# Performance work log

Measured on AMD Instinct MI355X. Metric: run time of the kernel, lower is better.

## Reference

```python
import jax, jax.numpy as jnp
import numpy as np

N_NODES = 100000
N_EDGES = 2000000
F_IN = 32
HID = 32
N_CLASS = 40


def _gru_cell(m, h, wih, whh, bih, bhh):
    # torch.nn.GRUCell math; wih/whh: [3H, H_in], gates ordered r, z, n
    gi = m @ wih.T + bih
    gh = h @ whh.T + bhh
    i_r, i_z, i_n = jnp.split(gi, 3, axis=-1)
    h_r, h_z, h_n = jnp.split(gh, 3, axis=-1)
    r = jax.nn.sigmoid(i_r + h_r)
    z = jax.nn.sigmoid(i_z + h_z)
    n = jnp.tanh(i_n + r * h_n)
    return (1.0 - z) * n + z * h


def _gated_conv(x, edge_index, edge_weight, w_proj, w_msg, wih, whh, bih, bhh):
    h = x @ w_proj                                   # [N, out]
    msg = (h @ w_msg)[edge_index[0]] * edge_weight[:, None]  # gather src -> [E, out]
    agg = jax.ops.segment_sum(msg, edge_index[1], num_segments=N_NODES)  # scatter-add to dst
    return _gru_cell(agg, h, wih, whh, bih, bhh)


def setup_inputs() -> dict:
    key = jax.random.key(0)
    ks = jax.random.split(key, 16)
    s = 0.1
    return {
        "x": jax.random.normal(ks[0], (N_NODES, F_IN), jnp.float32),
        "edge_index": jax.random.randint(ks[1], (2, N_EDGES), 0, N_NODES, jnp.int64),
        "edge_weight": jax.random.uniform(ks[2], (N_EDGES,), jnp.float32),
        "W1_proj": jax.random.normal(ks[3], (F_IN, HID), jnp.float32) * s,
        "W1_msg": jax.random.normal(ks[4], (HID, HID), jnp.float32) * s,
        "gru1_wih": jax.random.normal(ks[5], (3 * HID, HID), jnp.float32) * s,
        "gru1_whh": jax.random.normal(ks[6], (3 * HID, HID), jnp.float32) * s,
        "gru1_bih": jax.random.normal(ks[7], (3 * HID,), jnp.float32) * s,
        "gru1_bhh": jax.random.normal(ks[8], (3 * HID,), jnp.float32) * s,
        "W2_proj": jax.random.normal(ks[9], (HID, N_CLASS), jnp.float32) * s,
        "W2_msg": jax.random.normal(ks[10], (N_CLASS, N_CLASS), jnp.float32) * s,
        "gru2_wih": jax.random.normal(ks[11], (3 * N_CLASS, N_CLASS), jnp.float32) * s,
        "gru2_whh": jax.random.normal(ks[12], (3 * N_CLASS, N_CLASS), jnp.float32) * s,
        "gru2_bih": jax.random.normal(ks[13], (3 * N_CLASS,), jnp.float32) * s,
        "gru2_bhh": jax.random.normal(ks[14], (3 * N_CLASS,), jnp.float32) * s,
    }


def reference(x, edge_index, edge_weight, W1_proj, W1_msg, gru1_wih, gru1_whh,
              gru1_bih, gru1_bhh, W2_proj, W2_msg, gru2_wih, gru2_whh,
              gru2_bih, gru2_bhh):
    # eval mode: dropout is identity
    h = _gated_conv(x, edge_index, edge_weight, W1_proj, W1_msg,
                    gru1_wih, gru1_whh, gru1_bih, gru1_bhh)
    h = jax.nn.relu(h)
    h = _gated_conv(h, edge_index, edge_weight, W2_proj, W2_msg,
                    gru2_wih, gru2_whh, gru2_bih, gru2_bhh)
    return jax.nn.log_softmax(h, axis=-1)
```

## Files before the change

kernel.cpp:

```cpp
#include <hip/hip_runtime.h>
#include <math.h>

#define NN 100000
#define NE 2000000
#define FIN 32
#define H 32
#define NC 40

#define NBK 196
#define BSH 9
#define CAP 10880
#define EPT 16
#define EPB (256 * EPT)

#define NPROJ 12500
#define NCT1 10
#define NCT2 12
#define NWB 118

typedef _Float16 half_t;
typedef __attribute__((ext_vector_type(8))) _Float16 half8;
typedef __attribute__((ext_vector_type(4))) float f32x4;
typedef long long ll2 __attribute__((ext_vector_type(2)));

__device__ __forceinline__ float sigm_(float x) {
    return 1.0f / (1.0f + __expf(-x));
}
__device__ __forceinline__ float tanh_(float x) {
    x = fminf(fmaxf(x, -20.0f), 20.0f);
    float e = __expf(2.0f * x);
    return (e - 1.0f) / (e + 1.0f);
}

__device__ __forceinline__ void agg_run(int e, int e1, int q,
                                        const int2* __restrict__ evs,
                                        const half_t* __restrict__ src,
                                        float* acc) {
    const half8* s8 = (const half8*)src + q;
    const long long* ev8 = (const long long*)evs;
    if ((e & 1) && e < e1) {
        long long r = __builtin_nontemporal_load(ev8 + e);
        float w = __int_as_float((int)(r >> 32));
        half8 hv = s8[(size_t)(r & 0x1FFFF) * 4];
#pragma unroll
        for (int t = 0; t < 8; ++t) acc[t] += w * (float)hv[t];
        ++e;
    }
    int nfull = (e1 - e) >> 3;
    if (nfull > 0) {
        ll2 p0 = __builtin_nontemporal_load((const ll2*)(ev8 + e));
        ll2 p1 = __builtin_nontemporal_load((const ll2*)(ev8 + e + 2));
        ll2 p2 = __builtin_nontemporal_load((const ll2*)(ev8 + e + 4));
        ll2 p3 = __builtin_nontemporal_load((const ll2*)(ev8 + e + 6));
        for (int it = 1; it < nfull; ++it) {
            int en = e + it * 8;
            ll2 q0 = __builtin_nontemporal_load((const ll2*)(ev8 + en));
            ll2 q1 = __builtin_nontemporal_load((const ll2*)(ev8 + en + 2));
            ll2 q2 = __builtin_nontemporal_load((const ll2*)(ev8 + en + 4));
            ll2 q3 = __builtin_nontemporal_load((const ll2*)(ev8 + en + 6));
            half8 h0 = s8[(size_t)(p0[0] & 0x1FFFF) * 4];
            half8 h1 = s8[(size_t)(p0[1] & 0x1FFFF) * 4];
            half8 h2 = s8[(size_t)(p1[0] & 0x1FFFF) * 4];
            half8 h3 = s8[(size_t)(p1[1] & 0x1FFFF) * 4];
            half8 h4 = s8[(size_t)(p2[0] & 0x1FFFF) * 4];
            half8 h5 = s8[(size_t)(p2[1] & 0x1FFFF) * 4];
            half8 h6 = s8[(size_t)(p3[0] & 0x1FFFF) * 4];
            half8 h7 = s8[(size_t)(p3[1] & 0x1FFFF) * 4];
            float w0 = __int_as_float((int)(p0[0] >> 32));
            float w1 = __int_as_float((int)(p0[1] >> 32));
            float w2 = __int_as_float((int)(p1[0] >> 32));
            float w3 = __int_as_float((int)(p1[1] >> 32));
            float w4 = __int_as_float((int)(p2[0] >> 32));
            float w5 = __int_as_float((int)(p2[1] >> 32));
            float w6 = __int_as_float((int)(p3[0] >> 32));
            float w7 = __int_as_float((int)(p3[1] >> 32));
#pragma unroll
            for (int t = 0; t < 8; ++t) {
                acc[t] += w0 * (float)h0[t];
                acc[t] += w1 * (float)h1[t];
                acc[t] += w2 * (float)h2[t];
                acc[t] += w3 * (float)h3[t];
                acc[t] += w4 * (float)h4[t];
                acc[t] += w5 * (float)h5[t];
                acc[t] += w6 * (float)h6[t];
                acc[t] += w7 * (float)h7[t];
            }
            p0 = q0;
            p1 = q1;
            p2 = q2;
            p3 = q3;
        }
        {
            half8 h0 = s8[(size_t)(p0[0] & 0x1FFFF) * 4];
            half8 h1 = s8[(size_t)(p0[1] & 0x1FFFF) * 4];
            half8 h2 = s8[(size_t)(p1[0] & 0x1FFFF) * 4];
            half8 h3 = s8[(size_t)(p1[1] & 0x1FFFF) * 4];
            half8 h4 = s8[(size_t)(p2[0] & 0x1FFFF) * 4];
            half8 h5 = s8[(size_t)(p2[1] & 0x1FFFF) * 4];
            half8 h6 = s8[(size_t)(p3[0] & 0x1FFFF) * 4];
            half8 h7 = s8[(size_t)(p3[1] & 0x1FFFF) * 4];
            float w0 = __int_as_float((int)(p0[0] >> 32));
            float w1 = __int_as_float((int)(p0[1] >> 32));
            float w2 = __int_as_float((int)(p1[0] >> 32));
            float w3 = __int_as_float((int)(p1[1] >> 32));
            float w4 = __int_as_float((int)(p2[0] >> 32));
            float w5 = __int_as_float((int)(p2[1] >> 32));
            float w6 = __int_as_float((int)(p3[0] >> 32));
            float w7 = __int_as_float((int)(p3[1] >> 32));
#pragma unroll
            for (int t = 0; t < 8; ++t) {
                acc[t] += w0 * (float)h0[t];
                acc[t] += w1 * (float)h1[t];
                acc[t] += w2 * (float)h2[t];
                acc[t] += w3 * (float)h3[t];
                acc[t] += w4 * (float)h4[t];
                acc[t] += w5 * (float)h5[t];
                acc[t] += w6 * (float)h6[t];
                acc[t] += w7 * (float)h7[t];
            }
        }
        e += nfull * 8;
    }
    if (e + 4 <= e1) {
        ll2 p0 = __builtin_nontemporal_load((const ll2*)(ev8 + e));
        ll2 p1 = __builtin_nontemporal_load((const ll2*)(ev8 + e + 2));
        half8 h0 = s8[(size_t)(p0[0] & 0x1FFFF) * 4];
        half8 h1 = s8[(size_t)(p0[1] & 0x1FFFF) * 4];
        half8 h2 = s8[(size_t)(p1[0] & 0x1FFFF) * 4];
        half8 h3 = s8[(size_t)(p1[1] & 0x1FFFF) * 4];
        float w0 = __int_as_float((int)(p0[0] >> 32));
        float w1 = __int_as_float((int)(p0[1] >> 32));
        float w2 = __int_as_float((int)(p1[0] >> 32));
        float w3 = __int_as_float((int)(p1[1] >> 32));
#pragma unroll
        for (int t = 0; t < 8; ++t) {
            acc[t] += w0 * (float)h0[t];
            acc[t] += w1 * (float)h1[t];
            acc[t] += w2 * (float)h2[t];
            acc[t] += w3 * (float)h3[t];
        }
        e += 4;
    }
    if (e + 2 <= e1) {
        ll2 p0 = __builtin_nontemporal_load((const ll2*)(ev8 + e));
        half8 h0 = s8[(size_t)(p0[0] & 0x1FFFF) * 4];
        half8 h1 = s8[(size_t)(p0[1] & 0x1FFFF) * 4];
        float w0 = __int_as_float((int)(p0[0] >> 32));
        float w1 = __int_as_float((int)(p0[1] >> 32));
#pragma unroll
        for (int t = 0; t < 8; ++t) {
            acc[t] += w0 * (float)h0[t];
            acc[t] += w1 * (float)h1[t];
        }
        e += 2;
    }
    if (e < e1) {
        long long r = __builtin_nontemporal_load(ev8 + e);
        float w = __int_as_float((int)(r >> 32));
        half8 hv = s8[(size_t)(r & 0x1FFFF) * 4];
#pragma unroll
        for (int t = 0; t < 8; ++t) acc[t] += w * (float)hv[t];
    }
}

__global__ __launch_bounds__(256) void kA_bucket(const int* __restrict__ ei,
                                                 const float* __restrict__ ew,
                                                 int* __restrict__ gcur,
                                                 long long* __restrict__ rec) {
    __shared__ long long recs[EPB];
    __shared__ int gdst[EPB];
    __shared__ int cnt[NBK], base[NBK], sofs[NBK];
    __shared__ int ssc[256];
    int tid = threadIdx.x;
    for (int i = tid; i < NBK; i += 256) cnt[i] = 0;
    __syncthreads();
    int e0 = blockIdx.x * EPB;
    int dcache[EPT];
#pragma unroll
    for (int i = 0; i < EPT; ++i) {
        int e = e0 + i * 256 + tid;
        dcache[i] = (e < NE) ? ei[NE + e] : -1;
        if (e < NE) atomicAdd(&cnt[dcache[i] >> BSH], 1);
    }
    __syncthreads();
    int cv = (tid < NBK) ? cnt[tid] : 0;
    ssc[tid] = cv;
    __syncthreads();
    for (int off = 1; off < 256; off <<= 1) {
        int v = (tid >= off) ? ssc[tid - off] : 0;
        __syncthreads();
        ssc[tid] += v;
        __syncthreads();
    }
    if (tid < NBK) {
        sofs[tid] = ssc[tid] - cv;
        base[tid] = atomicAdd(&gcur[tid], cv);
        cnt[tid] = 0;
    }
    __syncthreads();
#pragma unroll
    for (int i = 0; i < EPT; ++i) {
        int e = e0 + i * 256 + tid;
        if (e < NE) {
            int d = dcache[i], s = ei[e];
            int b = d >> BSH;
            int r = atomicAdd(&cnt[b], 1);
            int slot = sofs[b] + r;
            int pos = base[b] + r;
            int lo = s | ((d & 511) << 17);
            recs[slot] = (long long)(unsigned)lo |
                         ((long long)__float_as_int(ew[e]) << 32);
            gdst[slot] = (pos < CAP) ? (b * CAP + pos) : -1;
        }
    }
    __syncthreads();
    int nrec = min(EPB, NE - e0);
    for (int i = tid; i < nrec; i += 256) {
        int gd = gdst[i];
        if (gd >= 0) rec[gd] = recs[i];
    }
}

__global__ __launch_bounds__(256) void kB_sort(const int* __restrict__ gcur,
                                               const int2* __restrict__ rec,
                                               int2* __restrict__ evs,
                                               int* __restrict__ ofs,
                                               int* __restrict__ ocn) {
    __shared__ int hist[2048], lofs[2048], ssc[256];
    int tid = threadIdx.x, b = blockIdx.x;
    int nb0 = b << BSH;
    int nnodes = min(512, NN - nb0);
    int cntb = min(gcur[b], CAP);
    for (int i = tid; i < 2048; i += 256) hist[i] = 0;
    __syncthreads();
    const int2* rb = rec + (size_t)b * CAP;
    for (int i = tid; i < cntb; i += 256) {
        int rx = rb[i].x;
        int bin = (((rx >> 17) & 511) << 2) | ((rx & 0x1FFFF) >> 15);
        atomicAdd(&hist[bin], 1);
    }
    __syncthreads();
    int base = tid * 8, ls = 0, lh[8];
#pragma unroll
    for (int j = 0; j < 8; ++j) {
        lh[j] = hist[base + j];
        ls += lh[j];
    }
    ssc[tid] = ls;
    __syncthreads();
    for (int off = 1; off < 256; off <<= 1) {
        int v = (tid >= off) ? ssc[tid - off] : 0;
        __syncthreads();
        ssc[tid] += v;
        __syncthreads();
    }
    int ex = ssc[tid] - ls;
#pragma unroll
    for (int j = 0; j < 8; ++j) {
        lofs[base + j] = ex;
        ex += lh[j];
    }
    __syncthreads();
    for (int l = tid; l < nnodes; l += 256) {
        int c = hist[4 * l] + hist[4 * l + 1] + hist[4 * l + 2] + hist[4 * l + 3];
        ofs[nb0 + l] = b * CAP + lofs[4 * l];
        ocn[nb0 + l] = c;
    }
    __syncthreads();
    for (int i = tid; i < 2048; i += 256) hist[i] = 0;
    __syncthreads();
    int2* eb = evs + (size_t)b * CAP;
    for (int i = tid; i < cntb; i += 256) {
        int2 r = rb[i];
        int bin = (((r.x >> 17) & 511) << 2) | ((r.x & 0x1FFFF) >> 15);
        int rk = atomicAdd(&hist[bin], 1);
        eb[lofs[bin] + rk] = make_int2(r.x & 0x1FFFF, r.y);
    }
}

__global__ __launch_bounds__(256) void k_prep(const float* __restrict__ x,
                                              const float* __restrict__ W1p,
                                              const float* __restrict__ W1m,
                                              const float* __restrict__ wih1,
                                              const float* __restrict__ whh1,
                                              const float* __restrict__ W2p,
                                              const float* __restrict__ W2m,
                                              const float* __restrict__ wih2,
                                              const float* __restrict__ whh2,
                                              half_t* __restrict__ Hd,
                                              half_t* __restrict__ W1sw,
                                              half_t* __restrict__ W2sw,
                                              half_t* __restrict__ W2pf,
                                              int* __restrict__ gcur) {
    __shared__ float sWp[FIN * H];
    __shared__ float sx[8][FIN];
    __shared__ float P2l[32 * NC];
    int b = blockIdx.x, tid = threadIdx.x;
    if (b < NPROJ) {
        for (int i = tid; i < FIN * H; i += 256) sWp[i] = W1p[i];
        int nb = b * 8;
        int nl = tid >> 5, j = tid & 31;
        int n = nb + nl;
        if (n < NN) sx[nl][j] = x[(size_t)n * FIN + j];
        __syncthreads();
        float acc = 0.f;
#pragma unroll
        for (int k = 0; k < FIN; ++k) acc += sx[nl][k] * sWp[k * H + j];
        if (n < NN) Hd[(size_t)n * 32 + j] = (half_t)acc;
        return;
    }
    int wb = b - NPROJ;
    if (wb == 0 && tid < NBK) gcur[tid] = 0;
    if (wb < 40) {
        int i = wb * 256 + tid;
        int j = i & 7, lane = (i >> 3) & 63;
        int rest = i >> 9;
        int ct = rest % NCT1, s = rest / NCT1;
        int k = s * 32 + (lane >> 4) * 8 + j;
        int col = ct * 16 + (lane & 15);
        int g = col >> 5, jj = col & 31;
        float v = 0.f;
        if (g <= 2) {
            if (k < 32) {
                float acc = 0.f;
#pragma unroll
                for (int t = 0; t < H; ++t) acc += W1m[k * H + t] * wih1[(g * H + jj) * H + t];
                v = acc;
            } else if (g < 2) {
                v = whh1[(g * H + jj) * H + (k - 32)];
            }
        } else if (g == 3) {
            if (k >= 32) v = whh1[(2 * H + jj) * H + (k - 32)];
        } else {
            if (k >= 32 && (k - 32) == jj) v = 1.f;
        }
        W1sw[i] = (half_t)v;
    } else if (wb < 112) {
        for (int e = tid; e < 32 * NC; e += 256) {
            int k = e / NC, t = e % NC;
            float a = 0.f;
#pragma unroll
            for (int u = 0; u < NC; ++u) a += W2p[k * NC + u] * W2m[u * NC + t];
            P2l[e] = a;
        }
        __syncthreads();
        int i2 = (wb - 40) * 256 + tid;
        int j = i2 & 7, lane = (i2 >> 3) & 63;
        int rest = i2 >> 9;
        int ct = rest % NCT2, s = rest / NCT2;
        int k = s * 32 + (lane >> 4) * 8 + j;
        int col = ct * 16 + (lane & 15);
        int g = col / 48, jj = col % 48;
        float v = 0.f;
        if (jj < NC) {
            if (g <= 2) {
                if (k < 32) {
                    float acc = 0.f;
#pragma unroll
                    for (int t = 0; t < NC; ++t)
                        acc += P2l[k * NC + t] * wih2[(g * NC + jj) * NC + t];
                    v = acc;
                } else if (k < 72 && g < 2) {
                    v = whh2[(g * NC + jj) * NC + (k - 32)];
                }
            } else {
                if (k >= 32 && k < 72) v = whh2[(2 * NC + jj) * NC + (k - 32)];
            }
        }
        W2sw[i2] = (half_t)v;
    } else {
        int i3 = (wb - 112) * 256 + tid;
        int j = i3 & 7, lane = (i3 >> 3) & 63, ct = i3 >> 9;
        int k = (lane >> 4) * 8 + j;
        int col = ct * 16 + (lane & 15);
        W2pf[i3] = (half_t)((col < NC) ? W2p[k * NC + col] : 0.f);
    }
}

__global__ __launch_bounds__(128, 4) void k_l1(const int* __restrict__ ofs,
                                               const int* __restrict__ ocn,
                                               const int2* __restrict__ evs,
                                               const half_t* __restrict__ Hd,
                                               const half8* __restrict__ W1sw,
                                               const float* __restrict__ bih,
                                               const float* __restrict__ bhh,
                                               half_t* __restrict__ Hh) {
    __shared__ half8 aggT[16][9];
    int tid = threadIdx.x;
    int n0 = blockIdx.x * 16;
    half8 a1;
    if (tid < 64) a1 = ((const half8*)Hd)[(size_t)(n0 + (tid & 15)) * 4 + (tid >> 4)];
    {
        int nl = tid >> 3, s = tid & 7, g = s >> 2, q = s & 3;
        int n = n0 + nl;
        int s0 = ofs[n], c = ocn[n];
        int c0 = (c + 1) >> 1;
        int eb = g ? (s0 + c0) : s0;
        int ee = g ? (s0 + c) : (s0 + c0);
        float acc[8] = {0.f, 0.f, 0.f, 0.f, 0.f, 0.f, 0.f, 0.f};
        agg_run(eb, ee, q, evs, Hd, acc);
        half8 o;
#pragma unroll
        for (int t = 0; t < 8; ++t) o[t] = (half_t)acc[t];
        aggT[nl][s] = o;
    }
    __syncthreads();
    if (tid >= 64) return;
    int lane = tid, m16 = lane & 15, qq = lane >> 4;
    half8 pa = aggT[m16][qq], pb = aggT[m16][4 + qq];
    half8 a0;
#pragma unroll
    for (int t = 0; t < 8; ++t) a0[t] = (half_t)((float)pa[t] + (float)pb[t]);
    f32x4 macc[NCT1];
#pragma unroll
    for (int ct = 0; ct < NCT1; ++ct) macc[ct] = (f32x4){0.f, 0.f, 0.f, 0.f};
#pragma unroll
    for (int ct = 0; ct < NCT1; ++ct) {
        macc[ct] = __builtin_amdgcn_mfma_f32_16x16x32_f16(a0, W1sw[ct * 64 + lane], macc[ct], 0, 0, 0);
        macc[ct] = __builtin_amdgcn_mfma_f32_16x16x32_f16(a1, W1sw[(NCT1 + ct) * 64 + lane], macc[ct], 0, 0, 0);
    }
#pragma unroll
    for (int ct = 0; ct < 2; ++ct) {
        int j = ct * 16 + m16;
        float br = bih[j] + bhh[j];
        float bz = bih[H + j] + bhh[H + j];
        float bi = bih[2 * H + j], bh = bhh[2 * H + j];
#pragma unroll
        for (int m = 0; m < 4; ++m) {
            int node = n0 + qq * 4 + m;
            float r = sigm_(macc[ct][m] + br);
            float z = sigm_(macc[2 + ct][m] + bz);
            float ng = tanh_(macc[4 + ct][m] + bi + r * (macc[6 + ct][m] + bh));
            float hj = macc[8 + ct][m];
            float o = fmaxf((1.f - z) * ng + z * hj, 0.f);
            Hh[(size_t)node * 32 + j] = (half_t)o;
        }
    }
}

__global__ __launch_bounds__(128, 4) void k_l2(const int* __restrict__ ofs,
                                               const int* __restrict__ ocn,
                                               const int2* __restrict__ evs,
                                               const half_t* __restrict__ Hh,
                                               const half8* __restrict__ W2sw,
                                               const half8* __restrict__ W2pf,
                                               const float* __restrict__ bih,
                                               const float* __restrict__ bhh,
                                               float* __restrict__ out) {
    __shared__ half8 aggT[16][9];
    __shared__ half_t h2c[16][72];
    int tid = threadIdx.x;
    int n0 = blockIdx.x * 16;
    if (tid < 64) {
        int lane = tid, m16 = lane & 15, qq = lane >> 4;
        half8 ah = ((const half8*)Hh)[(size_t)(n0 + m16) * 4 + qq];
        f32x4 hC[3];
#pragma unroll
        for (int ct = 0; ct < 3; ++ct) hC[ct] = (f32x4){0.f, 0.f, 0.f, 0.f};
#pragma unroll
        for (int ct = 0; ct < 3; ++ct)
            hC[ct] = __builtin_amdgcn_mfma_f32_16x16x32_f16(ah, W2pf[ct * 64 + lane], hC[ct], 0, 0, 0);
#pragma unroll
        for (int ct = 0; ct < 3; ++ct)
#pragma unroll
            for (int m = 0; m < 4; ++m)
                h2c[qq * 4 + m][ct * 16 + m16] = (half_t)hC[ct][m];
    } else {
        int t2 = tid - 64;
        for (int i5 = t2; i5 < 16 * 24; i5 += 64)
            h2c[i5 / 24][48 + i5 % 24] = (half_t)0.f;
    }
    {
        int nl = tid >> 3, s = tid & 7, g = s >> 2, q = s & 3;
        int n = n0 + nl;
        int s0 = ofs[n], c = ocn[n];
        int c0 = (c + 1) >> 1;
        int eb = g ? (s0 + c0) : s0;
        int ee = g ? (s0 + c) : (s0 + c0);
        float acc[8] = {0.f, 0.f, 0.f, 0.f, 0.f, 0.f, 0.f, 0.f};
        agg_run(eb, ee, q, evs, Hh, acc);
        half8 o;
#pragma unroll
        for (int t = 0; t < 8; ++t) o[t] = (half_t)acc[t];
        aggT[nl][s] = o;
    }
    __syncthreads();
    if (tid >= 64) return;
    int lane = tid, m16 = lane & 15, qq = lane >> 4;
    half8 pa = aggT[m16][qq], pb = aggT[m16][4 + qq];
    half8 a0;
#pragma unroll
    for (int t = 0; t < 8; ++t) a0[t] = (half_t)((float)pa[t] + (float)pb[t]);
    half8 a1 = *(const half8*)&h2c[m16][qq * 8];
    half8 a2 = *(const half8*)&h2c[m16][32 + qq * 8];
    f32x4 macc[NCT2];
#pragma unroll
    for (int ct = 0; ct < NCT2; ++ct) macc[ct] = (f32x4){0.f, 0.f, 0.f, 0.f};
#pragma unroll
    for (int ct = 0; ct < NCT2; ++ct) {
        macc[ct] = __builtin_amdgcn_mfma_f32_16x16x32_f16(a0, W2sw[ct * 64 + lane], macc[ct], 0, 0, 0);
        macc[ct] = __builtin_amdgcn_mfma_f32_16x16x32_f16(a1, W2sw[(NCT2 + ct) * 64 + lane], macc[ct], 0, 0, 0);
        macc[ct] = __builtin_amdgcn_mfma_f32_16x16x32_f16(a2, W2sw[(2 * NCT2 + ct) * 64 + lane], macc[ct], 0, 0, 0);
    }
    float v[3][4];
#pragma unroll
    for (int ct = 0; ct < 3; ++ct) {
        int j = ct * 16 + m16;
        int jc = (j < NC) ? j : (NC - 1);
        float br = bih[jc] + bhh[jc];
        float bz = bih[NC + jc] + bhh[NC + jc];
        float bi = bih[2 * NC + jc], bh = bhh[2 * NC + jc];
#pragma unroll
        for (int m = 0; m < 4; ++m) {
            float r = sigm_(macc[ct][m] + br);
            float z = sigm_(macc[3 + ct][m] + bz);
            float ng = tanh_(macc[6 + ct][m] + bi + r * (macc[9 + ct][m] + bh));
            float hj = (float)h2c[qq * 4 + m][jc];
            v[ct][m] = (1.f - z) * ng + z * hj;
        }
    }
    bool v2ok = (m16 < 8);
#pragma unroll
    for (int m = 0; m < 4; ++m) {
        float mx = fmaxf(v[0][m], v[1][m]);
        if (v2ok) mx = fmaxf(mx, v[2][m]);
#pragma unroll
        for (int d = 1; d < 16; d <<= 1) mx = fmaxf(mx, __shfl_xor(mx, d));
        float se = __expf(v[0][m] - mx) + __expf(v[1][m] - mx) +
                   (v2ok ? __expf(v[2][m] - mx) : 0.f);
#pragma unroll
        for (int d = 1; d < 16; d <<= 1) se += __shfl_xor(se, d);
        float ls = mx + __logf(se);
        int node = n0 + qq * 4 + m;
        out[(size_t)node * NC + m16] = v[0][m] - ls;
        out[(size_t)node * NC + 16 + m16] = v[1][m] - ls;
        if (v2ok) out[(size_t)node * NC + 32 + m16] = v[2][m] - ls;
    }
}

extern "C" void kernel_launch(void* const* d_in, const int* in_sizes, int n_in,
                              void* d_out, int out_size, void* d_ws, size_t ws_size,
                              hipStream_t stream) {
    const float* x = (const float*)d_in[0];
    const int* ei = (const int*)d_in[1];
    const float* ew = (const float*)d_in[2];
    const float* W1p = (const float*)d_in[3];
    const float* W1m = (const float*)d_in[4];
    const float* g1wih = (const float*)d_in[5];
    const float* g1whh = (const float*)d_in[6];
    const float* g1bih = (const float*)d_in[7];
    const float* g1bhh = (const float*)d_in[8];
    const float* W2p = (const float*)d_in[9];
    const float* W2m = (const float*)d_in[10];
    const float* g2wih = (const float*)d_in[11];
    const float* g2whh = (const float*)d_in[12];
    const float* g2bih = (const float*)d_in[13];
    const float* g2bhh = (const float*)d_in[14];
    float* ws = (float*)d_ws;

    long long* rec = (long long*)ws;
    int2* evs = (int2*)(ws + 4264960);
    half_t* Hd = (half_t*)(ws + 8529920);
    half_t* Hh = (half_t*)(ws + 10130176);
    int* ofs = (int*)(ws + 11730432);
    int* ocn = (int*)(ws + 11830432);
    int* gcur = (int*)(ws + 11930432);
    half_t* W1sw = (half_t*)(ws + 11930688);
    half_t* W2sw = W1sw + 10240;
    half_t* W2pf = W2sw + 18432;
    float* out = (float*)d_out;

    k_prep<<<NPROJ + NWB, 256, 0, stream>>>(x, W1p, W1m, g1wih, g1whh,
                                            W2p, W2m, g2wih, g2whh,
                                            Hd, W1sw, W2sw, W2pf, gcur);
    kA_bucket<<<(NE + EPB - 1) / EPB, 256, 0, stream>>>(ei, ew, gcur, rec);
    kB_sort<<<NBK, 256, 0, stream>>>(gcur, (const int2*)rec, evs, ofs, ocn);
    k_l1<<<NN / 16, 128, 0, stream>>>(ofs, ocn, evs, Hd, (const half8*)W1sw,
                                      g1bih, g1bhh, Hh);
    k_l2<<<NN / 16, 128, 0, stream>>>(ofs, ocn, evs, Hh, (const half8*)W2sw,
                                      (const half8*)W2pf, g2bih, g2bhh, out);
}
```

Before: 258.3 us.

## Sort nodes by in-degree within buckets to balance aggregation blocks

kB_sort now builds a per-bucket counting sort of nodes by in-degree (capped at 63) and writes a node permutation. k_l1 and k_l2 process nodes in that permuted order, so each 16-node block handles nodes of similar degree and threads waiting on long edge lists are reduced. The cost is an extra permutation array, indirect loads for node ids, and scattered output writes that lose contiguity.

After: 286.4 us. +10.9%, slower.

```diff
diff --git a/kernel.cpp b/kernel.cpp
--- a/kernel.cpp
+++ b/kernel.cpp
@@ -225,13 +225,19 @@
                                                const int2* __restrict__ rec,
                                                int2* __restrict__ evs,
                                                int* __restrict__ ofs,
-                                               int* __restrict__ ocn) {
+                                               int* __restrict__ ocn,
+                                               int* __restrict__ perm) {
     __shared__ int hist[2048], lofs[2048], ssc[256];
+    __shared__ int dh[64], dcur[64];
     int tid = threadIdx.x, b = blockIdx.x;
     int nb0 = b << BSH;
     int nnodes = min(512, NN - nb0);
     int cntb = min(gcur[b], CAP);
     for (int i = tid; i < 2048; i += 256) hist[i] = 0;
+    if (tid < 64) {
+        dh[tid] = 0;
+        dcur[tid] = 0;
+    }
     __syncthreads();
     const int2* rb = rec + (size_t)b * CAP;
     for (int i = tid; i < cntb; i += 256) {
@@ -265,6 +271,24 @@
         int c = hist[4 * l] + hist[4 * l + 1] + hist[4 * l + 2] + hist[4 * l + 3];
         ofs[nb0 + l] = b * CAP + lofs[4 * l];
         ocn[nb0 + l] = c;
+        atomicAdd(&dh[min(c, 63)], 1);
+    }
+    __syncthreads();
+    if (tid == 0) {
+        int run = 0;
+#pragma unroll
+        for (int d = 0; d < 64; ++d) {
+            int v = dh[d];
+            dh[d] = run;
+            run += v;
+        }
+    }
+    __syncthreads();
+    for (int l = tid; l < nnodes; l += 256) {
+        int c = hist[4 * l] + hist[4 * l + 1] + hist[4 * l + 2] + hist[4 * l + 3];
+        int d = min(c, 63);
+        int r = atomicAdd(&dcur[d], 1);
+        perm[nb0 + dh[d] + r] = nb0 + l;
     }
     __syncthreads();
     for (int i = tid; i < 2048; i += 256) hist[i] = 0;
@@ -380,19 +404,22 @@
 __global__ __launch_bounds__(128, 4) void k_l1(const int* __restrict__ ofs,
                                                const int* __restrict__ ocn,
                                                const int2* __restrict__ evs,
+                                               const int* __restrict__ perm,
                                                const half_t* __restrict__ Hd,
                                                const half8* __restrict__ W1sw,
                                                const float* __restrict__ bih,
                                                const float* __restrict__ bhh,
                                                half_t* __restrict__ Hh) {
     __shared__ half8 aggT[16][9];
+    __shared__ int sperm[16];
     int tid = threadIdx.x;
     int n0 = blockIdx.x * 16;
+    if (tid < 16) sperm[tid] = perm[n0 + tid];
     half8 a1;
-    if (tid < 64) a1 = ((const half8*)Hd)[(size_t)(n0 + (tid & 15)) * 4 + (tid >> 4)];
+    if (tid < 64) a1 = ((const half8*)Hd)[(size_t)perm[n0 + (tid & 15)] * 4 + (tid >> 4)];
     {
         int nl = tid >> 3, s = tid & 7, g = s >> 2, q = s & 3;
-        int n = n0 + nl;
+        int n = perm[n0 + nl];
         int s0 = ofs[n], c = ocn[n];
         int c0 = (c + 1) >> 1;
         int eb = g ? (s0 + c0) : s0;
@@ -427,7 +454,7 @@
         float bi = bih[2 * H + j], bh = bhh[2 * H + j];
 #pragma unroll
         for (int m = 0; m < 4; ++m) {
-            int node = n0 + qq * 4 + m;
+            int node = sperm[qq * 4 + m];
             float r = sigm_(macc[ct][m] + br);
             float z = sigm_(macc[2 + ct][m] + bz);
             float ng = tanh_(macc[4 + ct][m] + bi + r * (macc[6 + ct][m] + bh));
@@ -441,6 +468,7 @@
 __global__ __launch_bounds__(128, 4) void k_l2(const int* __restrict__ ofs,
                                                const int* __restrict__ ocn,
                                                const int2* __restrict__ evs,
+                                               const int* __restrict__ perm,
                                                const half_t* __restrict__ Hh,
                                                const half8* __restrict__ W2sw,
                                                const half8* __restrict__ W2pf,
@@ -449,11 +477,13 @@
                                                float* __restrict__ out) {
     __shared__ half8 aggT[16][9];
     __shared__ half_t h2c[16][72];
+    __shared__ int sperm[16];
     int tid = threadIdx.x;
     int n0 = blockIdx.x * 16;
+    if (tid < 16) sperm[tid] = perm[n0 + tid];
     if (tid < 64) {
         int lane = tid, m16 = lane & 15, qq = lane >> 4;
-        half8 ah = ((const half8*)Hh)[(size_t)(n0 + m16) * 4 + qq];
+        half8 ah = ((const half8*)Hh)[(size_t)perm[n0 + m16] * 4 + qq];
         f32x4 hC[3];
 #pragma unroll
         for (int ct = 0; ct < 3; ++ct) hC[ct] = (f32x4){0.f, 0.f, 0.f, 0.f};
@@ -472,7 +502,7 @@
     }
     {
         int nl = tid >> 3, s = tid & 7, g = s >> 2, q = s & 3;
-        int n = n0 + nl;
+        int n = perm[n0 + nl];
         int s0 = ofs[n], c = ocn[n];
         int c0 = (c + 1) >> 1;
         int eb = g ? (s0 + c0) : s0;
@@ -531,7 +561,7 @@
 #pragma unroll
         for (int d = 1; d < 16; d <<= 1) se += __shfl_xor(se, d);
         float ls = mx + __logf(se);
-        int node = n0 + qq * 4 + m;
+        int node = sperm[qq * 4 + m];
         out[(size_t)node * NC + m16] = v[0][m] - ls;
         out[(size_t)node * NC + 16 + m16] = v[1][m] - ls;
         if (v2ok) out[(size_t)node * NC + 32 + m16] = v[2][m] - ls;
@@ -565,7 +595,8 @@
     int* ofs = (int*)(ws + 11730432);
     int* ocn = (int*)(ws + 11830432);
     int* gcur = (int*)(ws + 11930432);
-    half_t* W1sw = (half_t*)(ws + 11930688);
+    int* perm = (int*)(ws + 11930688);
+    half_t* W1sw = (half_t*)(ws + 12030688);
     half_t* W2sw = W1sw + 10240;
     half_t* W2pf = W2sw + 18432;
     float* out = (float*)d_out;
@@ -574,9 +605,9 @@
                                             W2p, W2m, g2wih, g2whh,
                                             Hd, W1sw, W2sw, W2pf, gcur);
     kA_bucket<<<(NE + EPB - 1) / EPB, 256, 0, stream>>>(ei, ew, gcur, rec);
-    kB_sort<<<NBK, 256, 0, stream>>>(gcur, (const int2*)rec, evs, ofs, ocn);
-    k_l1<<<NN / 16, 128, 0, stream>>>(ofs, ocn, evs, Hd, (const half8*)W1sw,
+    kB_sort<<<NBK, 256, 0, stream>>>(gcur, (const int2*)rec, evs, ofs, ocn, perm);
+    k_l1<<<NN / 16, 128, 0, stream>>>(ofs, ocn, evs, perm, Hd, (const half8*)W1sw,
                                       g1bih, g1bhh, Hh);
-    k_l2<<<NN / 16, 128, 0, stream>>>(ofs, ocn, evs, Hh, (const half8*)W2sw,
+    k_l2<<<NN / 16, 128, 0, stream>>>(ofs, ocn, evs, perm, Hh, (const half8*)W2sw,
                                       (const half8*)W2pf, g2bih, g2bhh, out);
 }
```
